# Optimization experiments

Hardware: AMD Instinct MI355X
Metric: run time of the kernel (lower is better)

The kernel has to match this reference:

```python
import jax, jax.numpy as jnp
import numpy as np

WS, OWS, NH, DIM, MLP_H = 16, 24, 6, 180, 360
PAD = (OWS - WS) // 2
SCALE = (DIM // NH) ** -0.5


def _ln(x, w, b):
    m = jnp.mean(x, -1, keepdims=True)
    v = jnp.var(x, -1, keepdims=True)
    return (x - m) * jax.lax.rsqrt(v + 1e-5) * w + b


def _rpi():
    # relative position index between ordinary (WS) and extended (OWS) windows
    ci = np.stack(np.meshgrid(np.arange(WS), np.arange(WS), indexing='ij')).reshape(2, -1)
    ce = np.stack(np.meshgrid(np.arange(OWS), np.arange(OWS), indexing='ij')).reshape(2, -1)
    rel = (ce[:, None, :] - ci[:, :, None]).transpose(1, 2, 0) + (WS - 1)  # [WS^2, OWS^2, 2]
    rel[:, :, 0] *= WS + OWS - 1
    return jnp.asarray(rel.sum(-1), dtype=jnp.int32)  # values in [0, (WS+OWS-1)^2)


def setup_inputs():
    key = jax.random.key(0)
    ks = jax.random.split(key, 8)
    h = w = 256
    b = 1
    p = lambda k, shape: jax.random.normal(k, shape, jnp.float32) * 0.02
    return {
        'x': jax.random.normal(ks[0], (b, h * w, DIM), jnp.float32),
        'rpi': _rpi(),
        'norm1_w': jnp.ones((DIM,), jnp.float32), 'norm1_b': jnp.zeros((DIM,), jnp.float32),
        'qkv_w': p(ks[1], (DIM, 3 * DIM)), 'qkv_b': jnp.zeros((3 * DIM,), jnp.float32),
        'rpb': p(ks[2], ((WS + OWS - 1) ** 2, NH)),
        'proj_w': p(ks[3], (DIM, DIM)), 'proj_b': jnp.zeros((DIM,), jnp.float32),
        'norm2_w': jnp.ones((DIM,), jnp.float32), 'norm2_b': jnp.zeros((DIM,), jnp.float32),
        'fc1_w': p(ks[4], (DIM, MLP_H)), 'fc1_b': jnp.zeros((MLP_H,), jnp.float32),
        'fc2_w': p(ks[5], (MLP_H, DIM)), 'fc2_b': jnp.zeros((DIM,), jnp.float32),
        'h': h, 'w': w,
    }


def _ocab(x, rpi, norm1_w, norm1_b, qkv_w, qkv_b, rpb, proj_w, proj_b,
          norm2_w, norm2_b, fc1_w, fc1_b, fc2_w, fc2_b, h, w):
    b, L, c = x.shape
    nhw, nww = h // WS, w // WS
    nw = nhw * nww
    shortcut = x
    xn = _ln(x, norm1_w, norm1_b).reshape(b, h, w, c)
    qkv = xn @ qkv_w + qkv_b                      # [b,h,w,3c]
    q = qkv[..., :c]
    kv = jnp.moveaxis(qkv[..., c:], -1, 1)        # [b,2c,h,w]
    # non-overlapping query windows -> [b*nw, WS*WS, c]
    qw = q.reshape(b, nhw, WS, nww, WS, c).transpose(0, 1, 3, 2, 4, 5).reshape(b * nw, WS * WS, c)
    # overlapping KV windows (torch.nn.Unfold(kernel=OWS, stride=WS, pad=PAD) equivalent)
    kv_pad = jnp.pad(kv, ((0, 0), (0, 0), (PAD, PAD), (PAD, PAD)))
    rows = (jnp.arange(nhw) * WS)[:, None] + jnp.arange(OWS)   # [nhw, OWS]
    cols = (jnp.arange(nww) * WS)[:, None] + jnp.arange(OWS)   # [nww, OWS]
    kvw = kv_pad[:, :, rows][:, :, :, :, cols]    # [b,2c,nhw,OWS,nww,OWS]
    kvw = kvw.reshape(b, 2, c, nhw, OWS, nww, OWS)
    kvw = kvw.transpose(1, 0, 3, 5, 4, 6, 2).reshape(2, b * nw, OWS * OWS, c)
    k_w, v_w = kvw[0], kvw[1]
    B_, nq, n, d = b * nw, WS * WS, OWS * OWS, c // NH
    q_ = qw.reshape(B_, nq, NH, d).transpose(0, 2, 1, 3) * SCALE
    k_ = k_w.reshape(B_, n, NH, d).transpose(0, 2, 1, 3)
    v_ = v_w.reshape(B_, n, NH, d).transpose(0, 2, 1, 3)
    attn = jnp.einsum('bhqd,bhnd->bhqn', q_, k_)
    bias = rpb[rpi.reshape(-1)].reshape(nq, n, NH).transpose(2, 0, 1)  # [NH, nq, n]
    attn = jax.nn.softmax(attn + bias[None], axis=-1)
    out = jnp.einsum('bhqn,bhnd->bhqd', attn, v_).transpose(0, 2, 1, 3).reshape(B_, nq, c)
    # window reverse
    out = out.reshape(b, nhw, nww, WS, WS, c).transpose(0, 1, 3, 2, 4, 5).reshape(b, h * w, c)
    x = out @ proj_w + proj_b + shortcut
    xn2 = _ln(x, norm2_w, norm2_b)
    mlp = jax.nn.gelu(xn2 @ fc1_w + fc1_b, approximate=False) @ fc2_w + fc2_b
    return x + mlp


def reference(x, rpi, norm1_w, norm1_b, qkv_w, qkv_b, rpb, proj_w, proj_b,
              norm2_w, norm2_b, fc1_w, fc1_b, fc2_w, fc2_b, h, w):
    return _ocab(x, rpi, norm1_w, norm1_b, qkv_w, qkv_b, rpb, proj_w, proj_b,
                 norm2_w, norm2_b, fc1_w, fc1_b, fc2_w, fc2_b, h, w)
```

## Files before the change

kernel.cpp:

```cpp
#include <hip/hip_runtime.h>

typedef float f32x4 __attribute__((ext_vector_type(4)));
typedef float fvec4 __attribute__((ext_vector_type(4)));
typedef __bf16 bf16x8 __attribute__((ext_vector_type(8)));
typedef unsigned short u16;
typedef u16 u16x8 __attribute__((ext_vector_type(8)));
typedef u16 u16x4 __attribute__((ext_vector_type(4)));
typedef int i32x2 __attribute__((ext_vector_type(2)));

#define SCALE_Q 0.18257418583505536f
#define LOG2E   1.4426950408889634f
#define SCALE_Q2 (SCALE_Q * LOG2E)

__device__ __forceinline__ u16 f2bf(float f) {
    union { __bf16 h; u16 u; } cv; cv.h = (__bf16)f; return cv.u;
}
__device__ __forceinline__ float bf2f(u16 u) {
    union { __bf16 h; u16 u; } cv; cv.u = u; return (float)cv.h;
}
__device__ __forceinline__ float exp2_raw(float x) {
    float r;
    asm("v_exp_f32 %0, %1" : "=v"(r) : "v"(x));
    return r;
}
__device__ __forceinline__ unsigned pk_bf16(float a, float b) {
    unsigned r;
    asm("v_cvt_pk_bf16_f32 %0, %1, %2" : "=v"(r) : "v"(a), "v"(b));
    return r;
}

#define GLD16(gsrc, ldst) __builtin_amdgcn_global_load_lds( \
    (const __attribute__((address_space(1))) unsigned*)(gsrc), \
    (__attribute__((address_space(3))) unsigned*)(ldst), 16, 0, 0)

__device__ __forceinline__ void xswap16(int a, int b, int& u, int& v) {
#if __has_builtin(__builtin_amdgcn_permlane16_swap)
    i32x2 r = __builtin_amdgcn_permlane16_swap(a, b, false, false);
    u = r[0]; v = r[1];
#else
    int sa = __builtin_amdgcn_ds_swizzle(a, 0x401F);
    int sb = __builtin_amdgcn_ds_swizzle(b, 0x401F);
    bool hi = (threadIdx.x & 16) != 0;
    u = hi ? sb : a;
    v = hi ? b : sa;
#endif
}

__device__ __forceinline__ void border_yx(int i, int& y, int& x) {
    if (i < 1056)      { y = i / 264; x = i % 264; }
    else if (i < 2112) { int j = i - 1056; y = 260 + j / 264; x = j % 264; }
    else               { int j = i - 2112; y = 4 + (j >> 3); int xx = j & 7;
                         x = (xx < 4) ? xx : 256 + xx; }
}

__global__ __launch_bounds__(256)
void prepln_k(const float* __restrict__ x, const float* __restrict__ n1w,
              const float* __restrict__ n1b, u16* __restrict__ xn,
              const float* __restrict__ qkv_w, const float* __restrict__ proj_w,
              const float* __restrict__ fc1_w, const float* __restrict__ fc2_w,
              const int* __restrict__ rpi, const float* __restrict__ rpb,
              u16* __restrict__ qkvT, u16* __restrict__ projT,
              u16* __restrict__ fc1T, u16* __restrict__ fc2T,
              u16* __restrict__ bias5, unsigned* __restrict__ kp_u32,
              unsigned* __restrict__ vp_u32)
{
    if (blockIdx.x < 16384) {
        int row = blockIdx.x * 4 + (threadIdx.x >> 6);
        int lane = threadIdx.x & 63;
        fvec4 v = {0.f, 0.f, 0.f, 0.f};
        if (lane < 45) v = *(const fvec4*)(x + (long)row * 180 + lane * 4);
        float s  = v.x + v.y + v.z + v.w;
        float sq = v.x * v.x + v.y * v.y + v.z * v.z + v.w * v.w;
        for (int m = 1; m < 64; m <<= 1) { s += __shfl_xor(s, m); sq += __shfl_xor(sq, m); }
        float mean = s * (1.f / 180.f);
        float var  = sq * (1.f / 180.f) - mean * mean;
        float rstd = rsqrtf(var + 1e-5f);
        if (lane < 45) {
            u16x4 o;
            #pragma unroll
            for (int j = 0; j < 4; j++) {
                int c = lane * 4 + j;
                o[j] = f2bf((v[j] - mean) * rstd * n1w[c] + n1b[c]);
            }
            *(u16x4*)(xn + (long)row * 192 + lane * 4) = o;
        } else if (lane < 48) {
            u16x4 z = {0, 0, 0, 0};
            *(u16x4*)(xn + (long)row * 192 + 180 + (lane - 45) * 4) = z;
        }
        return;
    }
    int idx = (blockIdx.x - 16384) * 256 + threadIdx.x;
    if (idx < 122880) {
        int e = idx & 7, l15b = (idx >> 3) & 15, lgb = (idx >> 7) & 3;
        int kstep = (idx >> 9) % 6, ng = idx / 3072;
        int col = ng * 16 + l15b, kd = kstep * 32 + lgb * 8 + e;
        qkvT[idx] = (col < 540 && kd < 180) ? f2bf(qkv_w[kd * 540 + col]) : (u16)0;
    } else if (idx < 172032) {
        int i = idx - 122880;
        int e = i & 7, l15b = (i >> 3) & 15, lgb = (i >> 7) & 3;
        int kstep = (i >> 9) % 6, ng = i / 3072;
        int col = ng * 16 + l15b, kdp = kstep * 32 + lgb * 8 + e;
        int sub = kdp & 31;
        int k = (kdp >> 5) * 30 + sub;
        projT[i] = (col < 180 && sub < 30) ? f2bf(proj_w[k * 180 + col]) : (u16)0;
    } else if (idx < 245760) {
        int i = idx - 172032;
        int e = i & 7, l15b = (i >> 3) & 15, lgb = (i >> 7) & 3;
        int kstep = (i >> 9) % 6, ng = i / 3072;
        int col = ng * 16 + l15b, kd = kstep * 32 + lgb * 8 + e;
        fc1T[i] = (col < 360 && kd < 180) ? f2bf(fc1_w[kd * 360 + col]) : (u16)0;
    } else if (idx < 344064) {
        int i = idx - 245760;
        int e = i & 7, l15b = (i >> 3) & 15, lgb = (i >> 7) & 3;
        int kstep = (i >> 9) % 12, ng = i / 6144;
        int col = ng * 16 + l15b, kd = kstep * 32 + lgb * 8 + e;
        fc2T[i] = (col < 180 && kd < 360) ? f2bf(fc2_w[kd * 180 + col]) : (u16)0;
    } else if (idx < 1228800) {
        int i = idx - 344064;
        int e = i & 15, l15 = (i >> 4) & 15, wv2 = (i >> 8) & 3, lg2 = (i >> 10) & 3;
        int cm36 = i >> 12;
        int hh = cm36 / 36, cm = cm36 % 36;
        int ch = cm >> 2, mi = cm & 3;
        int ni = e >> 2, rr = e & 3;
        int q = wv2 * 64 + ni * 16 + l15;
        int key = ch * 64 + mi * 16 + lg2 * 4 + rr;
        bias5[i] = f2bf(rpb[rpi[q * 576 + key] * 6 + hh] * LOG2E);
    } else if (idx < 1628160) {
        int i = idx - 1228800;
        int tok = i >> 4, wj = i & 15;
        int h = tok / 4160, b = tok % 4160, y, xx;
        border_yx(b, y, xx);
        kp_u32[((h * 264 + y) * 264 + xx) * 16 + wj] = 0u;
    } else if (idx < 2021376) {
        int i = idx - 1628160;
        int h = i / 65536, t = i % 65536;
        int y = t >> 8, xx = t & 255;
        kp_u32[((h * 264 + y + 4) * 264 + xx + 4) * 16 + 15] = 0u;
    } else if (idx < 2236800) {
        int i = idx - 2021376;
        int h = i / 35904, r = i % 35904;
        vp_u32[(h * 32 + 30) * 35904 + r] = 0x3F803F80u;
    } else if (idx < 2452224) {
        int i = idx - 2236800;
        int h = i / 35904, r = i % 35904;
        vp_u32[(h * 32 + 31) * 35904 + r] = 0u;
    } else if (idx < 3016704) {
        int i = idx - 2452224;
        int hd = i / 3136, j = i % 3136;
        int h = hd / 30, d = hd % 30;
        int y, xu;
        if (j < 1088) { int r = j / 136; y = r + (r >= 4 ? 256 : 0); xu = j % 136; }
        else { int j2 = j - 1088; y = 4 + (j2 >> 3); int q = j2 & 7;
               xu = (q < 2) ? q : 128 + q; }
        vp_u32[((h * 32 + d) * 264 + y) * 136 + xu] = 0u;
    }
}

template<int KTOT, int NCB, int EPI>
__global__ __launch_bounds__(256)
void gemm_k(const u16* __restrict__ A, const u16* __restrict__ BtF,
            const float* __restrict__ bias, const float* __restrict__ resid,
            void* __restrict__ o0, void* __restrict__ o1, void* __restrict__ o2)
{
    constexpr int NKT = KTOT / 32;
    __shared__ u16 lds_a[128 * 192];
    const int tid = threadIdx.x;
    const int l = tid & 63, wv = tid >> 6;
    const int wm = wv >> 1, wn = wv & 1;
    const int l15 = l & 15, lg = l >> 4;
    const int rx7 = l15 & 7;
    const long rowb = (long)blockIdx.x * 128;
    const int cb0 = blockIdx.y * NCB;
    const f32x4 fz = {0.f, 0.f, 0.f, 0.f};

    f32x4 acc[4][2];
    #pragma unroll
    for (int i = 0; i < 4; i++) { acc[i][0] = fz; acc[i][1] = fz; }

    const u16* aptr[4];
    #pragma unroll
    for (int mi = 0; mi < 4; mi++)
        aptr[mi] = lds_a + (wm * 64 + mi * 16 + l15) * 192;

    auto epilogue = [&](int cb, f32x4 (&ac)[4][2]) {
        #pragma unroll
        for (int nd = 0; nd < 2; nd++) {
            const int c = cb * 64 + wn * 32 + nd * 16 + l15;
            if (EPI == 0) {
                if (c < 540) {
                    const float bb = bias[c];
                    const int sec = (c >= 360) ? 2 : ((c >= 180) ? 1 : 0);
                    const int cc = c - sec * 180;
                    const int hh = cc / 30, d = cc - hh * 30;
                    #pragma unroll
                    for (int mi = 0; mi < 4; mi++) {
                        const long t0 = rowb + wm * 64 + mi * 16 + lg * 4;
                        const int y = (int)(t0 >> 8), x0 = (int)(t0 & 255);
                        if (sec == 0) {
                            int win = ((y >> 4) << 4) | (x0 >> 4);
                            int qrow0 = ((y & 15) << 4) | (x0 & 15);
                            u16* dst = (u16*)o0 + (((long)(win * 6 + hh)) * 256 + qrow0) * 32 + d;
                            #pragma unroll
                            for (int rr = 0; rr < 4; rr++)
                                dst[rr * 32] = f2bf((ac[mi][nd][rr] + bb) * SCALE_Q2);
                        } else if (sec == 1) {
                            u16* dst = (u16*)o1 + (((long)hh * 264 + y + 4) * 264 + x0 + 4) * 32 + d;
                            #pragma unroll
                            for (int rr = 0; rr < 4; rr++)
                                dst[rr * 32] = f2bf(ac[mi][nd][rr] + bb);
                        } else {
                            long dstoff = (((long)hh * 32 + d) * 264 + y + 4) * 272 + x0 + 4;
                            union { u16x4 v4; unsigned u2[2]; } pv;
                            pv.u2[0] = pk_bf16(ac[mi][nd][0] + bb, ac[mi][nd][1] + bb);
                            pv.u2[1] = pk_bf16(ac[mi][nd][2] + bb, ac[mi][nd][3] + bb);
                            *(u16x4*)((u16*)o2 + dstoff) = pv.v4;
                        }
                    }
                }
            } else {
                if (c < 180) {
                    const float bb = bias[c];
                    #pragma unroll
                    for (int mi = 0; mi < 4; mi++) {
                        const long t0 = rowb + wm * 64 + mi * 16 + lg * 4;
                        const float* rs = resid + t0 * 180 + c;
                        u16* dst = (u16*)o0 + t0 * 192 + c;
                        #pragma unroll
                        for (int rr = 0; rr < 4; rr++)
                            dst[rr * 192] = f2bf(ac[mi][nd][rr] + bb + rs[rr * 180]);
                    }
                } else {
                    #pragma unroll
                    for (int mi = 0; mi < 4; mi++) {
                        const long t0 = rowb + wm * 64 + mi * 16 + lg * 4;
                        u16* dst = (u16*)o0 + t0 * 192 + c;
                        #pragma unroll
                        for (int rr = 0; rr < 4; rr++)
                            dst[rr * 192] = 0;
                    }
                }
            }
        }
    };

    #pragma unroll
    for (int R = 0; R < 12; ++R) {
        int idx = R * 256 + tid;
        int row = idx / 24, gp = idx - row * 24;
        int g = (gp & 24) | ((gp & 7) ^ (row & 7));
        GLD16(A + (rowb + row) * KTOT + g * 8,
              (char*)lds_a + R * 4096 + wv * 1024);
    }
    __syncthreads();

    #pragma unroll
    for (int icb = 0; icb < NCB; ++icb) {
        const u16* Bf = BtF + ((long)((cb0 + icb) * 4 + wn * 2) * NKT) * 512 + l * 8;
        #pragma unroll
        for (int kg = 0; kg < 6; kg += 3) {
            bf16x8 bfr[2][3];
            #pragma unroll
            for (int g2 = 0; g2 < 3; ++g2) {
                bfr[0][g2] = *(const bf16x8*)(Bf + (kg + g2) * 512);
                bfr[1][g2] = *(const bf16x8*)(Bf + (NKT + kg + g2) * 512);
            }
            #pragma unroll
            for (int g2 = 0; g2 < 3; ++g2) {
                const int k = kg + g2;
                const int gk = k * 4 + lg;
                const int gpk = (gk & 24) | ((gk & 7) ^ rx7);
                bf16x8 af[4];
                #pragma unroll
                for (int mi = 0; mi < 4; mi++)
                    af[mi] = *(const bf16x8*)(aptr[mi] + gpk * 8);
                #pragma unroll
                for (int mi = 0; mi < 4; mi++)
                    #pragma unroll
                    for (int nd = 0; nd < 2; nd++)
                        acc[mi][nd] = __builtin_amdgcn_mfma_f32_16x16x32_bf16(af[mi], bfr[nd][g2], acc[mi][nd], 0, 0, 0);
            }
        }
        epilogue(cb0 + icb, acc);
        #pragma unroll
        for (int i = 0; i < 4; i++) { acc[i][0] = fz; acc[i][1] = fz; }
    }
}

__global__ __launch_bounds__(256)
void mlp_k(const u16* __restrict__ x2b, const u16* __restrict__ fc1T,
           const u16* __restrict__ fc2T, const float* __restrict__ b1,
           const float* __restrict__ b2, const float* __restrict__ n2w,
           const float* __restrict__ n2b, float* __restrict__ out)
{
    __shared__ u16 lds_a[64 * 192];
    __shared__ u16 H[64 * 384];
    const int tid = threadIdx.x;
    const int l = tid & 63, wv = tid >> 6;
    const int l15 = l & 15, lg = l >> 4;
    const int rx7 = l15 & 7;
    const long rowb = (long)blockIdx.x * 64;
    const f32x4 fz = {0.f, 0.f, 0.f, 0.f};

    #pragma unroll
    for (int R = 0; R < 6; ++R) {
        int idx = R * 256 + tid;
        int row = idx / 24, gp = idx - row * 24;
        int g = (gp & 24) | ((gp & 7) ^ (row & 7));
        GLD16(x2b + (rowb + row) * 192 + g * 8, (char*)lds_a + R * 4096 + wv * 1024);
    }
    __syncthreads();

    {
        const int row = tid >> 2, q = tid & 3;
        const int rw7 = row & 7;
        u16* rbase = lds_a + row * 192;
        u16x8 vals[6];
        float s = 0.f, sq = 0.f;
        #pragma unroll
        for (int j = 0; j < 6; ++j) {
            int g = q * 6 + j;
            int pg = (g & 24) | ((g & 7) ^ rw7);
            vals[j] = *(const u16x8*)(rbase + pg * 8);
            #pragma unroll
            for (int e = 0; e < 8; ++e) {
                float v = bf2f(vals[j][e]);
                s += v; sq += v * v;
            }
        }
        s  += __shfl_xor(s, 1);  sq += __shfl_xor(sq, 1);
        s  += __shfl_xor(s, 2);  sq += __shfl_xor(sq, 2);
        float mean = s * (1.f / 180.f);
        float var  = sq * (1.f / 180.f) - mean * mean;
        float rstd = rsqrtf(var + 1e-5f);
        #pragma unroll
        for (int j = 0; j < 6; ++j) {
            int g = q * 6 + j;
            int pg = (g & 24) | ((g & 7) ^ rw7);
            u16x8 o;
            #pragma unroll
            for (int e = 0; e < 8; ++e) {
                int c = g * 8 + e;
                int cc = (c < 180) ? c : 0;
                float v = bf2f(vals[j][e]);
                float nv = (v - mean) * rstd * n2w[cc] + n2b[cc];
                o[e] = (c < 180) ? f2bf(nv) : (u16)0;
            }
            *(u16x8*)(rbase + pg * 8) = o;
        }
    }
    __syncthreads();

    const u16* aptr[4];
    #pragma unroll
    for (int mi = 0; mi < 4; mi++)
        aptr[mi] = lds_a + (mi * 16 + l15) * 192;

    #pragma unroll
    for (int cb = 0; cb < 6; ++cb) {
        f32x4 ac[4] = {fz, fz, fz, fz};
        const u16* Bf = fc1T + ((long)(cb * 4 + wv) * 6) * 512 + l * 8;
        #pragma unroll
        for (int k = 0; k < 6; ++k) {
            bf16x8 bfr = *(const bf16x8*)(Bf + k * 512);
            const int gk = k * 4 + lg;
            const int gpk = (gk & 24) | ((gk & 7) ^ rx7);
            bf16x8 af[4];
            #pragma unroll
            for (int mi = 0; mi < 4; mi++)
                af[mi] = *(const bf16x8*)(aptr[mi] + gpk * 8);
            #pragma unroll
            for (int mi = 0; mi < 4; mi++)
                ac[mi] = __builtin_amdgcn_mfma_f32_16x16x32_bf16(af[mi], bfr, ac[mi], 0, 0, 0);
        }
        const int c = cb * 64 + wv * 16 + l15;
        const float bb = (c < 360) ? b1[c] : 0.f;
        const int gC = c >> 3, cL = c & 7;
        #pragma unroll
        for (int mi = 0; mi < 4; mi++) {
            #pragma unroll
            for (int rr = 0; rr < 4; rr++) {
                int row = mi * 16 + lg * 4 + rr;
                float xx = ac[mi][rr] + bb;
                float u2n = -2.f * xx * (0.7978845608f + 0.0356774081f * xx * xx);
                float ge = xx / (1.f + __expf(u2n));
                int gS = (gC & ~7) | ((gC & 7) ^ (row & 7));
                H[row * 384 + gS * 8 + cL] = f2bf(ge);
            }
        }
    }
    __syncthreads();

    #pragma unroll
    for (int cb = 0; cb < 3; ++cb) {
        f32x4 ac[4] = {fz, fz, fz, fz};
        const u16* Bf = fc2T + ((long)(cb * 4 + wv) * 12) * 512 + l * 8;
        #pragma unroll
        for (int k = 0; k < 12; ++k) {
            bf16x8 bfr = *(const bf16x8*)(Bf + k * 512);
            const int gk = k * 4 + lg;
            const int gS = (gk & ~7) | ((gk & 7) ^ rx7);
            bf16x8 af[4];
            #pragma unroll
            for (int mi = 0; mi < 4; mi++)
                af[mi] = *(const bf16x8*)(H + (mi * 16 + l15) * 384 + gS * 8);
            #pragma unroll
            for (int mi = 0; mi < 4; mi++)
                ac[mi] = __builtin_amdgcn_mfma_f32_16x16x32_bf16(af[mi], bfr, ac[mi], 0, 0, 0);
        }
        const int c = cb * 64 + wv * 16 + l15;
        if (c < 180) {
            const float bb = b2[c];
            #pragma unroll
            for (int mi = 0; mi < 4; mi++) {
                const long t0 = rowb + mi * 16 + lg * 4;
                const u16* rs = x2b + t0 * 192 + c;
                float* dst = out + t0 * 180 + c;
                #pragma unroll
                for (int rr = 0; rr < 4; rr++)
                    dst[rr * 180] = ac[mi][rr] + bb + bf2f(rs[rr * 192]);
            }
        }
    }
}

__global__ __launch_bounds__(256)
void attn_k(const u16* __restrict__ q_g, const u16* __restrict__ K_pad,
            const u16* __restrict__ vP, const u16* __restrict__ bias5,
            u16* __restrict__ attn_out)
{
    __shared__ u16 kc[2][64 * 32];
    __shared__ u16 vt[2][32 * 64];

    const int w = ((blockIdx.x & 7) << 5) | (blockIdx.x >> 3);
    const int h = blockIdx.y;
    const int wy = w >> 4, wx = w & 15;
    const int tid = threadIdx.x;
    const int wv = tid >> 6, l = tid & 63;
    const int l15 = l & 15, lg = l >> 4;
    const int swzk = (l15 >> 1) & 3;
    const int swzv = l15 & 7;

    bf16x8 qb[4];
    #pragma unroll
    for (int ni = 0; ni < 4; ni++) {
        int qrow = wv * 64 + ni * 16 + l15;
        qb[ni] = *(const bf16x8*)(q_g + (((long)(w * 6 + h)) * 256 + qrow) * 32 + lg * 8);
    }

    f32x4 acc[2][4];
    #pragma unroll
    for (int i = 0; i < 2; i++)
        #pragma unroll
        for (int j = 0; j < 4; j++) acc[i][j] = (f32x4){0.f, 0.f, 0.f, 0.f};

    const int tK = tid >> 2;
    const int gtk = (l & 3) ^ ((l >> 3) & 3);
    const int aK = (tK >= 48) ? 2 : (tK >= 24 ? 1 : 0);
    const int bK = tK - aK * 24;
    const u16* KbaseRow = K_pad + (((long)(h * 264 + wy * 16)) * 264 + wx * 16) * 32 + gtk * 8;
    const int dV = tid >> 3;
    const int gtv = (l & 7) ^ (l >> 3);
    const int aV = gtv / 3, bV = (gtv % 3) * 8;
    const u16* Vrow0 = vP + ((((long)h * 32 + dV) * 264) + wy * 16) * 272 + wx * 16;
    const u16* Bp = bias5 + (long)h * 147456 + ((lg * 4 + wv) * 16 + l15) * 16;

    GLD16(KbaseRow + ((long)aK * 264 + bK) * 32, (char*)kc[0] + wv * 1024);
    GLD16(Vrow0 + aV * 272 + bV, (char*)vt[0] + wv * 1024);

    u16x8 bl[4], bh[4];
    #pragma unroll
    for (int mi = 0; mi < 4; mi++) {
        bl[mi] = *(const u16x8*)(Bp + mi * 4096);
        bh[mi] = *(const u16x8*)(Bp + mi * 4096 + 8);
    }

    #pragma unroll
    for (int ch = 0; ch < 9; ++ch) {
        __syncthreads();
        u16x8 bln[4], bhn[4];
        if (ch < 8) {
            int n = (ch + 1) * 64;
            int c1 = n / 24, c2 = n - c1 * 24;
            int bb2 = bK + c2;
            int t2 = bb2 >= 24;
            int oy = c1 + aK + t2, ox = bb2 - (t2 ? 24 : 0);
            GLD16(KbaseRow + ((long)oy * 264 + ox) * 32, (char*)kc[(ch + 1) & 1] + wv * 1024);
            int bbv = bV + c2;
            int t2v = bbv >= 24;
            int oyv = c1 + aV + t2v, oxv = bbv - (t2v ? 24 : 0);
            GLD16(Vrow0 + oyv * 272 + oxv, (char*)vt[(ch + 1) & 1] + wv * 1024);
            #pragma unroll
            for (int mi = 0; mi < 4; mi++) {
                bln[mi] = *(const u16x8*)(Bp + ((ch + 1) * 4 + mi) * 4096);
                bhn[mi] = *(const u16x8*)(Bp + ((ch + 1) * 4 + mi) * 4096 + 8);
            }
        }
        const u16* kcur = kc[ch & 1];
        const u16* vcur = vt[ch & 1];

        #pragma unroll
        for (int ks = 0; ks < 2; ++ks) {
            int Wp[2][4][2];
            #pragma unroll
            for (int mih = 0; mih < 2; ++mih) {
                int mi = ks * 2 + mih;
                int key = ks * 32 + mih * 16 + l15;
                bf16x8 ka = *(const bf16x8*)(kcur + key * 32 + (lg ^ swzk) * 8);
                union { u16x8 v; unsigned d[4]; } ulo, uhi;
                ulo.v = bl[mi]; uhi.v = bh[mi];
                f32x4 s[4];
                #pragma unroll
                for (int ni = 0; ni < 4; ni++) {
                    unsigned dA = (ni < 2) ? ulo.d[(ni & 1) * 2]     : uhi.d[(ni & 1) * 2];
                    unsigned dB = (ni < 2) ? ulo.d[(ni & 1) * 2 + 1] : uhi.d[(ni & 1) * 2 + 1];
                    f32x4 ci;
                    ci[0] = __uint_as_float(dA << 16);
                    ci[1] = __uint_as_float(dA & 0xFFFF0000u);
                    ci[2] = __uint_as_float(dB << 16);
                    ci[3] = __uint_as_float(dB & 0xFFFF0000u);
                    s[ni] = ci;
                }
                #pragma unroll
                for (int ni = 0; ni < 4; ni++)
                    s[ni] = __builtin_amdgcn_mfma_f32_16x16x32_bf16(ka, qb[ni], s[ni], 0, 0, 0);
                #pragma unroll
                for (int ni = 0; ni < 4; ni++) {
                    float p0 = exp2_raw(s[ni][0]);
                    float p1 = exp2_raw(s[ni][1]);
                    float p2 = exp2_raw(s[ni][2]);
                    float p3 = exp2_raw(s[ni][3]);
                    Wp[mih][ni][0] = (int)pk_bf16(p0, p1);
                    Wp[mih][ni][1] = (int)pk_bf16(p2, p3);
                }
            }
            bf16x8 va0 = *(const bf16x8*)(vcur + l15 * 64 + ((ks * 4 + lg) ^ swzv) * 8);
            bf16x8 va1 = *(const bf16x8*)(vcur + (16 + l15) * 64 + ((ks * 4 + lg) ^ swzv) * 8);
            #pragma unroll
            for (int ni = 0; ni < 4; ni++) {
                i32x2 r0 = __builtin_amdgcn_permlane32_swap(Wp[0][ni][0], Wp[1][ni][0], false, false);
                i32x2 r1 = __builtin_amdgcn_permlane32_swap(Wp[0][ni][1], Wp[1][ni][1], false, false);
                int wd0, wd1, wd2, wd3;
                xswap16(r0[0], r0[1], wd0, wd2);
                xswap16(r1[0], r1[1], wd1, wd3);
                union { int wd[4]; bf16x8 v; } pu;
                pu.wd[0] = wd0; pu.wd[1] = wd1; pu.wd[2] = wd2; pu.wd[3] = wd3;
                acc[0][ni] = __builtin_amdgcn_mfma_f32_16x16x32_bf16(va0, pu.v, acc[0][ni], 0, 0, 0);
                acc[1][ni] = __builtin_amdgcn_mfma_f32_16x16x32_bf16(va1, pu.v, acc[1][ni], 0, 0, 0);
            }
        }
        if (ch < 8) {
            #pragma unroll
            for (int mi = 0; mi < 4; mi++) { bl[mi] = bln[mi]; bh[mi] = bhn[mi]; }
        }
    }

    #pragma unroll
    for (int ni = 0; ni < 4; ni++) {
        float sum = __shfl(acc[1][ni][2], 48 + l15);
        float inv = 1.f / sum;
        int q = wv * 64 + ni * 16 + l15;
        int y = wy * 16 + (q >> 4), x = wx * 16 + (q & 15);
        u16* bp = attn_out + ((long)(y * 256 + x)) * 192 + h * 32;
        *(unsigned*)(bp + lg * 4)     = pk_bf16(acc[0][ni][0] * inv, acc[0][ni][1] * inv);
        *(unsigned*)(bp + lg * 4 + 2) = pk_bf16(acc[0][ni][2] * inv, acc[0][ni][3] * inv);
        if (lg < 3) {
            *(unsigned*)(bp + 16 + lg * 4)     = pk_bf16(acc[1][ni][0] * inv, acc[1][ni][1] * inv);
            *(unsigned*)(bp + 16 + lg * 4 + 2) = pk_bf16(acc[1][ni][2] * inv, acc[1][ni][3] * inv);
        } else {
            *(unsigned*)(bp + 28) = pk_bf16(acc[1][ni][0] * inv, acc[1][ni][1] * inv);
            *(unsigned*)(bp + 30) = 0u;
        }
    }
}

extern "C" void kernel_launch(void* const* d_in, const int* in_sizes, int n_in,
                              void* d_out, int out_size, void* d_ws, size_t ws_size,
                              hipStream_t stream)
{
    (void)in_sizes; (void)n_in; (void)out_size; (void)ws_size;
    const float* x      = (const float*)d_in[0];
    const int*   rpi    = (const int*)d_in[1];
    const float* n1w    = (const float*)d_in[2];
    const float* n1b    = (const float*)d_in[3];
    const float* qkv_w  = (const float*)d_in[4];
    const float* qkv_b  = (const float*)d_in[5];
    const float* rpb    = (const float*)d_in[6];
    const float* proj_w = (const float*)d_in[7];
    const float* proj_b = (const float*)d_in[8];
    const float* n2w    = (const float*)d_in[9];
    const float* n2b    = (const float*)d_in[10];
    const float* fc1_w  = (const float*)d_in[11];
    const float* fc1_b  = (const float*)d_in[12];
    const float* fc2_w  = (const float*)d_in[13];
    const float* fc2_b  = (const float*)d_in[14];
    float* out = (float*)d_out;

    char* ws = (char*)d_ws;
    size_t off = 0;
    auto alloc = [&](size_t bytes) -> void* {
        void* p = ws + off; off += (bytes + 511) & ~(size_t)511; return p;
    };
    u16*   xn     = (u16*)alloc(65536ull * 192 * 2);
    u16*   q_g    = (u16*)alloc(65536ull * 192 * 2);
    u16*   K_pad  = (u16*)alloc(6ull * 264 * 264 * 32 * 2);
    u16*   x2b    = (u16*)alloc(65536ull * 192 * 2);
    u16*   vP     = (u16*)alloc(6ull * 32 * 264 * 272 * 2);
    u16*   bias5  = (u16*)alloc(6ull * 36 * 4 * 4 * 16 * 16 * 2);
    u16*   qkvT   = (u16*)alloc(640ull * 192 * 2);
    u16*   projT  = (u16*)alloc(256ull * 192 * 2);
    u16*   fc1T   = (u16*)alloc(384ull * 192 * 2);
    u16*   fc2T   = (u16*)alloc(256ull * 384 * 2);
    u16*   ao     = xn;

    prepln_k<<<dim3(28168), dim3(256), 0, stream>>>(x, n1w, n1b, xn,
        qkv_w, proj_w, fc1_w, fc2_w, rpi, rpb,
        qkvT, projT, fc1T, fc2T, bias5, (unsigned*)K_pad, (unsigned*)vP);
    gemm_k<192, 3, 0><<<dim3(512, 3), dim3(256), 0, stream>>>(
        xn, qkvT, qkv_b, (const float*)nullptr, q_g, K_pad, vP);
    attn_k<<<dim3(256, 6), dim3(256), 0, stream>>>(q_g, K_pad, vP, bias5, ao);
    gemm_k<192, 3, 1><<<dim3(512, 1), dim3(256), 0, stream>>>(
        ao, projT, proj_b, x, x2b, nullptr, nullptr);
    mlp_k<<<dim3(1024), dim3(256), 0, stream>>>(
        x2b, fc1T, fc2T, fc1_b, fc2_b, n2w, n2b, out);
}
```

Measured before the change: 209.9 us.

## Split MLP hidden dim into halves and stage two KV chunks per barrier

The MLP kernel now computes the fc1+GELU hidden activations in two 192-wide halves and accumulates fc2 partial products into persistent registers. This halves the H shared buffer, which may allow more resident blocks, at the cost of an extra barrier and more accumulator registers. The attention kernel now loads two 64-key K/V chunks per stage into doubled LDS buffers. This halves the number of __syncthreads in the chunk loop, but bias prefetching is dropped and bias is now loaded inline per chunk, and LDS use in attn_k grows.

```diff
diff --git a/kernel.cpp b/kernel.cpp
--- a/kernel.cpp
+++ b/kernel.cpp
@@ -293,7 +293,7 @@
            const float* __restrict__ n2b, float* __restrict__ out)
 {
     __shared__ u16 lds_a[64 * 192];
-    __shared__ u16 H[64 * 384];
+    __shared__ u16 H[64 * 192];
     const int tid = threadIdx.x;
     const int l = tid & 63, wv = tid >> 6;
     const int l15 = l & 15, lg = l >> 4;
@@ -355,58 +355,72 @@
     for (int mi = 0; mi < 4; mi++)
         aptr[mi] = lds_a + (mi * 16 + l15) * 192;
 
-    #pragma unroll
-    for (int cb = 0; cb < 6; ++cb) {
-        f32x4 ac[4] = {fz, fz, fz, fz};
-        const u16* Bf = fc1T + ((long)(cb * 4 + wv) * 6) * 512 + l * 8;
-        #pragma unroll
-        for (int k = 0; k < 6; ++k) {
-            bf16x8 bfr = *(const bf16x8*)(Bf + k * 512);
-            const int gk = k * 4 + lg;
-            const int gpk = (gk & 24) | ((gk & 7) ^ rx7);
-            bf16x8 af[4];
-            #pragma unroll
-            for (int mi = 0; mi < 4; mi++)
-                af[mi] = *(const bf16x8*)(aptr[mi] + gpk * 8);
-            #pragma unroll
-            for (int mi = 0; mi < 4; mi++)
-                ac[mi] = __builtin_amdgcn_mfma_f32_16x16x32_bf16(af[mi], bfr, ac[mi], 0, 0, 0);
-        }
-        const int c = cb * 64 + wv * 16 + l15;
-        const float bb = (c < 360) ? b1[c] : 0.f;
-        const int gC = c >> 3, cL = c & 7;
-        #pragma unroll
-        for (int mi = 0; mi < 4; mi++) {
-            #pragma unroll
-            for (int rr = 0; rr < 4; rr++) {
-                int row = mi * 16 + lg * 4 + rr;
-                float xx = ac[mi][rr] + bb;
-                float u2n = -2.f * xx * (0.7978845608f + 0.0356774081f * xx * xx);
-                float ge = xx / (1.f + __expf(u2n));
-                int gS = (gC & ~7) | ((gC & 7) ^ (row & 7));
-                H[row * 384 + gS * 8 + cL] = f2bf(ge);
-            }
-        }
-    }
-    __syncthreads();
+    f32x4 acc2[3][4];
+    #pragma unroll
+    for (int cb = 0; cb < 3; ++cb)
+        #pragma unroll
+        for (int mi = 0; mi < 4; mi++) acc2[cb][mi] = fz;
+
+    #pragma unroll
+    for (int hk = 0; hk < 2; ++hk) {
+        if (hk) __syncthreads();
+        #pragma unroll
+        for (int cb = 0; cb < 3; ++cb) {
+            const int cbg = hk * 3 + cb;
+            f32x4 ac[4] = {fz, fz, fz, fz};
+            const u16* Bf = fc1T + ((long)(cbg * 4 + wv) * 6) * 512 + l * 8;
+            #pragma unroll
+            for (int k = 0; k < 6; ++k) {
+                bf16x8 bfr = *(const bf16x8*)(Bf + k * 512);
+                const int gk = k * 4 + lg;
+                const int gpk = (gk & 24) | ((gk & 7) ^ rx7);
+                bf16x8 af[4];
+                #pragma unroll
+                for (int mi = 0; mi < 4; mi++)
+                    af[mi] = *(const bf16x8*)(aptr[mi] + gpk * 8);
+                #pragma unroll
+                for (int mi = 0; mi < 4; mi++)
+                    ac[mi] = __builtin_amdgcn_mfma_f32_16x16x32_bf16(af[mi], bfr, ac[mi], 0, 0, 0);
+            }
+            const int cg = cbg * 64 + wv * 16 + l15;
+            const int cl = cb * 64 + wv * 16 + l15;
+            const float bb = (cg < 360) ? b1[cg] : 0.f;
+            const int gC = cl >> 3, cL = cl & 7;
+            #pragma unroll
+            for (int mi = 0; mi < 4; mi++) {
+                #pragma unroll
+                for (int rr = 0; rr < 4; rr++) {
+                    int row = mi * 16 + lg * 4 + rr;
+                    float xx = ac[mi][rr] + bb;
+                    float u2n = -2.f * xx * (0.7978845608f + 0.0356774081f * xx * xx);
+                    float ge = xx / (1.f + __expf(u2n));
+                    int gS = (gC & ~7) | ((gC & 7) ^ (row & 7));
+                    H[row * 192 + gS * 8 + cL] = f2bf(ge);
+                }
+            }
+        }
+        __syncthreads();
+        #pragma unroll
+        for (int cb = 0; cb < 3; ++cb) {
+            const u16* Bf = fc2T + ((long)(cb * 4 + wv) * 12 + hk * 6) * 512 + l * 8;
+            #pragma unroll
+            for (int k = 0; k < 6; ++k) {
+                bf16x8 bfr = *(const bf16x8*)(Bf + k * 512);
+                const int gk = k * 4 + lg;
+                const int gS = (gk & 24) | ((gk & 7) ^ rx7);
+                bf16x8 af[4];
+                #pragma unroll
+                for (int mi = 0; mi < 4; mi++)
+                    af[mi] = *(const bf16x8*)(H + (mi * 16 + l15) * 192 + gS * 8);
+                #pragma unroll
+                for (int mi = 0; mi < 4; mi++)
+                    acc2[cb][mi] = __builtin_amdgcn_mfma_f32_16x16x32_bf16(af[mi], bfr, acc2[cb][mi], 0, 0, 0);
+            }
+        }
+    }
 
     #pragma unroll
     for (int cb = 0; cb < 3; ++cb) {
-        f32x4 ac[4] = {fz, fz, fz, fz};
-        const u16* Bf = fc2T + ((long)(cb * 4 + wv) * 12) * 512 + l * 8;
-        #pragma unroll
-        for (int k = 0; k < 12; ++k) {
-            bf16x8 bfr = *(const bf16x8*)(Bf + k * 512);
-            const int gk = k * 4 + lg;
-            const int gS = (gk & ~7) | ((gk & 7) ^ rx7);
-            bf16x8 af[4];
-            #pragma unroll
-            for (int mi = 0; mi < 4; mi++)
-                af[mi] = *(const bf16x8*)(H + (mi * 16 + l15) * 384 + gS * 8);
-            #pragma unroll
-            for (int mi = 0; mi < 4; mi++)
-                ac[mi] = __builtin_amdgcn_mfma_f32_16x16x32_bf16(af[mi], bfr, ac[mi], 0, 0, 0);
-        }
         const int c = cb * 64 + wv * 16 + l15;
         if (c < 180) {
             const float bb = b2[c];
@@ -417,7 +431,7 @@
                 float* dst = out + t0 * 180 + c;
                 #pragma unroll
                 for (int rr = 0; rr < 4; rr++)
-                    dst[rr * 180] = ac[mi][rr] + bb + bf2f(rs[rr * 192]);
+                    dst[rr * 180] = acc2[cb][mi][rr] + bb + bf2f(rs[rr * 192]);
             }
         }
     }
@@ -428,8 +442,8 @@
             const u16* __restrict__ vP, const u16* __restrict__ bias5,
             u16* __restrict__ attn_out)
 {
-    __shared__ u16 kc[2][64 * 32];
-    __shared__ u16 vt[2][32 * 64];
+    __shared__ u16 kc[2][128 * 32];
+    __shared__ u16 vt[2][128 * 32];
 
     const int w = ((blockIdx.x & 7) << 5) | (blockIdx.x >> 3);
     const int h = blockIdx.y;
@@ -464,93 +478,92 @@
     const u16* Vrow0 = vP + ((((long)h * 32 + dV) * 264) + wy * 16) * 272 + wx * 16;
     const u16* Bp = bias5 + (long)h * 147456 + ((lg * 4 + wv) * 16 + l15) * 16;
 
-    GLD16(KbaseRow + ((long)aK * 264 + bK) * 32, (char*)kc[0] + wv * 1024);
-    GLD16(Vrow0 + aV * 272 + bV, (char*)vt[0] + wv * 1024);
-
-    u16x8 bl[4], bh[4];
-    #pragma unroll
-    for (int mi = 0; mi < 4; mi++) {
-        bl[mi] = *(const u16x8*)(Bp + mi * 4096);
-        bh[mi] = *(const u16x8*)(Bp + mi * 4096 + 8);
-    }
-
-    #pragma unroll
-    for (int ch = 0; ch < 9; ++ch) {
+    auto stageKV = [&](int cc, int buf, int s) {
+        int n = cc * 64;
+        int c1 = n / 24, c2 = n - c1 * 24;
+        int bb2 = bK + c2;
+        int t2 = bb2 >= 24;
+        int oy = c1 + aK + t2, ox = bb2 - (t2 ? 24 : 0);
+        GLD16(KbaseRow + ((long)oy * 264 + ox) * 32,
+              (char*)kc[buf] + s * 4096 + wv * 1024);
+        int bbv = bV + c2;
+        int t2v = bbv >= 24;
+        int oyv = c1 + aV + t2v, oxv = bbv - (t2v ? 24 : 0);
+        GLD16(Vrow0 + oyv * 272 + oxv,
+              (char*)vt[buf] + s * 4096 + wv * 1024);
+    };
+
+    stageKV(0, 0, 0);
+    stageKV(1, 0, 1);
+
+    #pragma unroll
+    for (int r = 0; r < 5; ++r) {
         __syncthreads();
-        u16x8 bln[4], bhn[4];
-        if (ch < 8) {
-            int n = (ch + 1) * 64;
-            int c1 = n / 24, c2 = n - c1 * 24;
-            int bb2 = bK + c2;
-            int t2 = bb2 >= 24;
-            int oy = c1 + aK + t2, ox = bb2 - (t2 ? 24 : 0);
-            GLD16(KbaseRow + ((long)oy * 264 + ox) * 32, (char*)kc[(ch + 1) & 1] + wv * 1024);
-            int bbv = bV + c2;
-            int t2v = bbv >= 24;
-            int oyv = c1 + aV + t2v, oxv = bbv - (t2v ? 24 : 0);
-            GLD16(Vrow0 + oyv * 272 + oxv, (char*)vt[(ch + 1) & 1] + wv * 1024);
+        if (2 * r + 2 < 9) stageKV(2 * r + 2, (r + 1) & 1, 0);
+        if (2 * r + 3 < 9) stageKV(2 * r + 3, (r + 1) & 1, 1);
+
+        #pragma unroll
+        for (int s = 0; s < 2; ++s) {
+            const int cc = 2 * r + s;
+            if (cc >= 9) break;
+            const u16* kcur = kc[r & 1] + s * 2048;
+            const u16* vcur = vt[r & 1] + s * 2048;
+            u16x8 bl[4], bh[4];
             #pragma unroll
             for (int mi = 0; mi < 4; mi++) {
-                bln[mi] = *(const u16x8*)(Bp + ((ch + 1) * 4 + mi) * 4096);
-                bhn[mi] = *(const u16x8*)(Bp + ((ch + 1) * 4 + mi) * 4096 + 8);
-            }
-        }
-        const u16* kcur = kc[ch & 1];
-        const u16* vcur = vt[ch & 1];
-
-        #pragma unroll
-        for (int ks = 0; ks < 2; ++ks) {
-            int Wp[2][4][2];
-            #pragma unroll
-            for (int mih = 0; mih < 2; ++mih) {
-                int mi = ks * 2 + mih;
-                int key = ks * 32 + mih * 16 + l15;
-                bf16x8 ka = *(const bf16x8*)(kcur + key * 32 + (lg ^ swzk) * 8);
-                union { u16x8 v; unsigned d[4]; } ulo, uhi;
-                ulo.v = bl[mi]; uhi.v = bh[mi];
-                f32x4 s[4];
+                bl[mi] = *(const u16x8*)(Bp + (cc * 4 + mi) * 4096);
+                bh[mi] = *(const u16x8*)(Bp + (cc * 4 + mi) * 4096 + 8);
+            }
+            #pragma unroll
+            for (int ks = 0; ks < 2; ++ks) {
+                int Wp[2][4][2];
+                #pragma unroll
+                for (int mih = 0; mih < 2; ++mih) {
+                    int mi = ks * 2 + mih;
+                    int key = ks * 32 + mih * 16 + l15;
+                    bf16x8 ka = *(const bf16x8*)(kcur + key * 32 + (lg ^ swzk) * 8);
+                    union { u16x8 v; unsigned d[4]; } ulo, uhi;
+                    ulo.v = bl[mi]; uhi.v = bh[mi];
+                    f32x4 ss[4];
+                    #pragma unroll
+                    for (int ni = 0; ni < 4; ni++) {
+                        unsigned dA = (ni < 2) ? ulo.d[(ni & 1) * 2]     : uhi.d[(ni & 1) * 2];
+                        unsigned dB = (ni < 2) ? ulo.d[(ni & 1) * 2 + 1] : uhi.d[(ni & 1) * 2 + 1];
+                        f32x4 ci;
+                        ci[0] = __uint_as_float(dA << 16);
+                        ci[1] = __uint_as_float(dA & 0xFFFF0000u);
+                        ci[2] = __uint_as_float(dB << 16);
+                        ci[3] = __uint_as_float(dB & 0xFFFF0000u);
+                        ss[ni] = ci;
+                    }
+                    #pragma unroll
+                    for (int ni = 0; ni < 4; ni++)
+                        ss[ni] = __builtin_amdgcn_mfma_f32_16x16x32_bf16(ka, qb[ni], ss[ni], 0, 0, 0);
+                    #pragma unroll
+                    for (int ni = 0; ni < 4; ni++) {
+                        float p0 = exp2_raw(ss[ni][0]);
+                        float p1 = exp2_raw(ss[ni][1]);
+                        float p2 = exp2_raw(ss[ni][2]);
+                        float p3 = exp2_raw(ss[ni][3]);
+                        Wp[mih][ni][0] = (int)pk_bf16(p0, p1);
+                        Wp[mih][ni][1] = (int)pk_bf16(p2, p3);
+                    }
+                }
+                bf16x8 va0 = *(const bf16x8*)(vcur + l15 * 64 + ((ks * 4 + lg) ^ swzv) * 8);
+                bf16x8 va1 = *(const bf16x8*)(vcur + (16 + l15) * 64 + ((ks * 4 + lg) ^ swzv) * 8);
                 #pragma unroll
                 for (int ni = 0; ni < 4; ni++) {
-                    unsigned dA = (ni < 2) ? ulo.d[(ni & 1) * 2]     : uhi.d[(ni & 1) * 2];
-                    unsigned dB = (ni < 2) ? ulo.d[(ni & 1) * 2 + 1] : uhi.d[(ni & 1) * 2 + 1];
-                    f32x4 ci;
-                    ci[0] = __uint_as_float(dA << 16);
-                    ci[1] = __uint_as_float(dA & 0xFFFF0000u);
-                    ci[2] = __uint_as_float(dB << 16);
-                    ci[3] = __uint_as_float(dB & 0xFFFF0000u);
-                    s[ni] = ci;
+                    i32x2 r0 = __builtin_amdgcn_permlane32_swap(Wp[0][ni][0], Wp[1][ni][0], false, false);
+                    i32x2 r1 = __builtin_amdgcn_permlane32_swap(Wp[0][ni][1], Wp[1][ni][1], false, false);
+                    int wd0, wd1, wd2, wd3;
+                    xswap16(r0[0], r0[1], wd0, wd2);
+                    xswap16(r1[0], r1[1], wd1, wd3);
+                    union { int wd[4]; bf16x8 v; } pu;
+                    pu.wd[0] = wd0; pu.wd[1] = wd1; pu.wd[2] = wd2; pu.wd[3] = wd3;
+                    acc[0][ni] = __builtin_amdgcn_mfma_f32_16x16x32_bf16(va0, pu.v, acc[0][ni], 0, 0, 0);
+                    acc[1][ni] = __builtin_amdgcn_mfma_f32_16x16x32_bf16(va1, pu.v, acc[1][ni], 0, 0, 0);
                 }
-                #pragma unroll
-                for (int ni = 0; ni < 4; ni++)
-                    s[ni] = __builtin_amdgcn_mfma_f32_16x16x32_bf16(ka, qb[ni], s[ni], 0, 0, 0);
-                #pragma unroll
-                for (int ni = 0; ni < 4; ni++) {
-                    float p0 = exp2_raw(s[ni][0]);
-                    float p1 = exp2_raw(s[ni][1]);
-                    float p2 = exp2_raw(s[ni][2]);
-                    float p3 = exp2_raw(s[ni][3]);
-                    Wp[mih][ni][0] = (int)pk_bf16(p0, p1);
-                    Wp[mih][ni][1] = (int)pk_bf16(p2, p3);
-                }
-            }
-            bf16x8 va0 = *(const bf16x8*)(vcur + l15 * 64 + ((ks * 4 + lg) ^ swzv) * 8);
-            bf16x8 va1 = *(const bf16x8*)(vcur + (16 + l15) * 64 + ((ks * 4 + lg) ^ swzv) * 8);
-            #pragma unroll
-            for (int ni = 0; ni < 4; ni++) {
-                i32x2 r0 = __builtin_amdgcn_permlane32_swap(Wp[0][ni][0], Wp[1][ni][0], false, false);
-                i32x2 r1 = __builtin_amdgcn_permlane32_swap(Wp[0][ni][1], Wp[1][ni][1], false, false);
-                int wd0, wd1, wd2, wd3;
-                xswap16(r0[0], r0[1], wd0, wd2);
-                xswap16(r1[0], r1[1], wd1, wd3);
-                union { int wd[4]; bf16x8 v; } pu;
-                pu.wd[0] = wd0; pu.wd[1] = wd1; pu.wd[2] = wd2; pu.wd[3] = wd3;
-                acc[0][ni] = __builtin_amdgcn_mfma_f32_16x16x32_bf16(va0, pu.v, acc[0][ni], 0, 0, 0);
-                acc[1][ni] = __builtin_amdgcn_mfma_f32_16x16x32_bf16(va1, pu.v, acc[1][ni], 0, 0, 0);
-            }
-        }
-        if (ch < 8) {
-            #pragma unroll
-            for (int mi = 0; mi < 4; mi++) { bl[mi] = bln[mi]; bh[mi] = bhn[mi]; }
+            }
         }
     }
 
```

New measurement: 239.6 us. +14.1%, slower.

## Fuse output projection and residual add into the MLP kernel

Applied to the files above, without the earlier changes.

Drops the separate projection GEMM launch and computes attn_out@proj_w + bias + shortcut inside mlp_k. The result is written straight to LDS as the LN2/fc1 input, and the residual is kept in registers for the final add. This removes the x2b global round trip and one kernel launch. In exchange, LDS is repartitioned into three 64x192 buffers with the GELU hidden tile split across two of them, and register pressure rises from holding the residual.

```diff
diff --git a/kernel.cpp b/kernel.cpp
--- a/kernel.cpp
+++ b/kernel.cpp
@@ -156,10 +156,10 @@
     }
 }
 
-template<int KTOT, int NCB, int EPI>
+template<int KTOT, int NCB>
 __global__ __launch_bounds__(256)
 void gemm_k(const u16* __restrict__ A, const u16* __restrict__ BtF,
-            const float* __restrict__ bias, const float* __restrict__ resid,
+            const float* __restrict__ bias,
             void* __restrict__ o0, void* __restrict__ o1, void* __restrict__ o2)
 {
     constexpr int NKT = KTOT / 32;
@@ -186,57 +186,33 @@
         #pragma unroll
         for (int nd = 0; nd < 2; nd++) {
             const int c = cb * 64 + wn * 32 + nd * 16 + l15;
-            if (EPI == 0) {
-                if (c < 540) {
-                    const float bb = bias[c];
-                    const int sec = (c >= 360) ? 2 : ((c >= 180) ? 1 : 0);
-                    const int cc = c - sec * 180;
-                    const int hh = cc / 30, d = cc - hh * 30;
-                    #pragma unroll
-                    for (int mi = 0; mi < 4; mi++) {
-                        const long t0 = rowb + wm * 64 + mi * 16 + lg * 4;
-                        const int y = (int)(t0 >> 8), x0 = (int)(t0 & 255);
-                        if (sec == 0) {
-                            int win = ((y >> 4) << 4) | (x0 >> 4);
-                            int qrow0 = ((y & 15) << 4) | (x0 & 15);
-                            u16* dst = (u16*)o0 + (((long)(win * 6 + hh)) * 256 + qrow0) * 32 + d;
-                            #pragma unroll
-                            for (int rr = 0; rr < 4; rr++)
-                                dst[rr * 32] = f2bf((ac[mi][nd][rr] + bb) * SCALE_Q2);
-                        } else if (sec == 1) {
-                            u16* dst = (u16*)o1 + (((long)hh * 264 + y + 4) * 264 + x0 + 4) * 32 + d;
-                            #pragma unroll
-                            for (int rr = 0; rr < 4; rr++)
-                                dst[rr * 32] = f2bf(ac[mi][nd][rr] + bb);
-                        } else {
-                            long dstoff = (((long)hh * 32 + d) * 264 + y + 4) * 272 + x0 + 4;
-                            union { u16x4 v4; unsigned u2[2]; } pv;
-                            pv.u2[0] = pk_bf16(ac[mi][nd][0] + bb, ac[mi][nd][1] + bb);
-                            pv.u2[1] = pk_bf16(ac[mi][nd][2] + bb, ac[mi][nd][3] + bb);
-                            *(u16x4*)((u16*)o2 + dstoff) = pv.v4;
-                        }
-                    }
-                }
-            } else {
-                if (c < 180) {
-                    const float bb = bias[c];
-                    #pragma unroll
-                    for (int mi = 0; mi < 4; mi++) {
-                        const long t0 = rowb + wm * 64 + mi * 16 + lg * 4;
-                        const float* rs = resid + t0 * 180 + c;
-                        u16* dst = (u16*)o0 + t0 * 192 + c;
+            if (c < 540) {
+                const float bb = bias[c];
+                const int sec = (c >= 360) ? 2 : ((c >= 180) ? 1 : 0);
+                const int cc = c - sec * 180;
+                const int hh = cc / 30, d = cc - hh * 30;
+                #pragma unroll
+                for (int mi = 0; mi < 4; mi++) {
+                    const long t0 = rowb + wm * 64 + mi * 16 + lg * 4;
+                    const int y = (int)(t0 >> 8), x0 = (int)(t0 & 255);
+                    if (sec == 0) {
+                        int win = ((y >> 4) << 4) | (x0 >> 4);
+                        int qrow0 = ((y & 15) << 4) | (x0 & 15);
+                        u16* dst = (u16*)o0 + (((long)(win * 6 + hh)) * 256 + qrow0) * 32 + d;
                         #pragma unroll
                         for (int rr = 0; rr < 4; rr++)
-                            dst[rr * 192] = f2bf(ac[mi][nd][rr] + bb + rs[rr * 180]);
-                    }
-                } else {
-                    #pragma unroll
-                    for (int mi = 0; mi < 4; mi++) {
-                        const long t0 = rowb + wm * 64 + mi * 16 + lg * 4;
-                        u16* dst = (u16*)o0 + t0 * 192 + c;
+                            dst[rr * 32] = f2bf((ac[mi][nd][rr] + bb) * SCALE_Q2);
+                    } else if (sec == 1) {
+                        u16* dst = (u16*)o1 + (((long)hh * 264 + y + 4) * 264 + x0 + 4) * 32 + d;
                         #pragma unroll
                         for (int rr = 0; rr < 4; rr++)
-                            dst[rr * 192] = 0;
+                            dst[rr * 32] = f2bf(ac[mi][nd][rr] + bb);
+                    } else {
+                        long dstoff = (((long)hh * 32 + d) * 264 + y + 4) * 272 + x0 + 4;
+                        union { u16x4 v4; unsigned u2[2]; } pv;
+                        pv.u2[0] = pk_bf16(ac[mi][nd][0] + bb, ac[mi][nd][1] + bb);
+                        pv.u2[1] = pk_bf16(ac[mi][nd][2] + bb, ac[mi][nd][3] + bb);
+                        *(u16x4*)((u16*)o2 + dstoff) = pv.v4;
                     }
                 }
             }
@@ -287,13 +263,16 @@
 }
 
 __global__ __launch_bounds__(256)
-void mlp_k(const u16* __restrict__ x2b, const u16* __restrict__ fc1T,
-           const u16* __restrict__ fc2T, const float* __restrict__ b1,
-           const float* __restrict__ b2, const float* __restrict__ n2w,
-           const float* __restrict__ n2b, float* __restrict__ out)
+void mlp_k(const u16* __restrict__ ao, const u16* __restrict__ projT,
+           const u16* __restrict__ fc1T, const u16* __restrict__ fc2T,
+           const float* __restrict__ pb, const float* __restrict__ b1,
+           const float* __restrict__ b2, const float* __restrict__ xres,
+           const float* __restrict__ n2w, const float* __restrict__ n2b,
+           float* __restrict__ out)
 {
-    __shared__ u16 lds_a[64 * 192];
-    __shared__ u16 H[64 * 384];
+    __shared__ u16 buf0[64 * 192];
+    __shared__ u16 x2bL[64 * 192];
+    __shared__ u16 buf2[64 * 192];
     const int tid = threadIdx.x;
     const int l = tid & 63, wv = tid >> 6;
     const int l15 = l & 15, lg = l >> 4;
@@ -306,14 +285,63 @@
         int idx = R * 256 + tid;
         int row = idx / 24, gp = idx - row * 24;
         int g = (gp & 24) | ((gp & 7) ^ (row & 7));
-        GLD16(x2b + (rowb + row) * 192 + g * 8, (char*)lds_a + R * 4096 + wv * 1024);
+        GLD16(ao + (rowb + row) * 192 + g * 8, (char*)buf0 + R * 4096 + wv * 1024);
+    }
+    __syncthreads();
+
+    const u16* aptr0[4];
+    #pragma unroll
+    for (int mi = 0; mi < 4; mi++)
+        aptr0[mi] = buf0 + (mi * 16 + l15) * 192;
+
+    unsigned resid[3][4][2];
+    #pragma unroll
+    for (int cb = 0; cb < 3; ++cb) {
+        f32x4 ac[4] = {fz, fz, fz, fz};
+        const u16* Bf = projT + ((long)(cb * 4 + wv) * 6) * 512 + l * 8;
+        #pragma unroll
+        for (int k = 0; k < 6; ++k) {
+            bf16x8 bfr = *(const bf16x8*)(Bf + k * 512);
+            const int gk = k * 4 + lg;
+            const int gpk = (gk & 24) | ((gk & 7) ^ rx7);
+            bf16x8 af[4];
+            #pragma unroll
+            for (int mi = 0; mi < 4; mi++)
+                af[mi] = *(const bf16x8*)(aptr0[mi] + gpk * 8);
+            #pragma unroll
+            for (int mi = 0; mi < 4; mi++)
+                ac[mi] = __builtin_amdgcn_mfma_f32_16x16x32_bf16(af[mi], bfr, ac[mi], 0, 0, 0);
+        }
+        const int c = cb * 64 + wv * 16 + l15;
+        const bool valid = (c < 180);
+        const float bb = valid ? pb[c] : 0.f;
+        const int g = c >> 3, e = c & 7;
+        #pragma unroll
+        for (int mi = 0; mi < 4; mi++) {
+            const long t0 = rowb + mi * 16 + lg * 4;
+            float v[4];
+            #pragma unroll
+            for (int rr = 0; rr < 4; rr++)
+                v[rr] = valid ? (ac[mi][rr] + bb + xres[(t0 + rr) * 180 + c]) : 0.f;
+            unsigned p0 = pk_bf16(v[0], v[1]);
+            unsigned p1 = pk_bf16(v[2], v[3]);
+            resid[cb][mi][0] = p0;
+            resid[cb][mi][1] = p1;
+            #pragma unroll
+            for (int rr = 0; rr < 4; rr++) {
+                int row = mi * 16 + lg * 4 + rr;
+                int gS = (g & 24) | ((g & 7) ^ (row & 7));
+                unsigned pw = (rr < 2) ? p0 : p1;
+                x2bL[row * 192 + gS * 8 + e] = (u16)((pw >> ((rr & 1) * 16)) & 0xFFFF);
+            }
+        }
     }
     __syncthreads();
 
     {
         const int row = tid >> 2, q = tid & 3;
         const int rw7 = row & 7;
-        u16* rbase = lds_a + row * 192;
+        u16* rbase = x2bL + row * 192;
         u16x8 vals[6];
         float s = 0.f, sq = 0.f;
         #pragma unroll
@@ -353,7 +381,7 @@
     const u16* aptr[4];
     #pragma unroll
     for (int mi = 0; mi < 4; mi++)
-        aptr[mi] = lds_a + (mi * 16 + l15) * 192;
+        aptr[mi] = x2bL + (mi * 16 + l15) * 192;
 
     #pragma unroll
     for (int cb = 0; cb < 6; ++cb) {
@@ -374,7 +402,9 @@
         }
         const int c = cb * 64 + wv * 16 + l15;
         const float bb = (c < 360) ? b1[c] : 0.f;
-        const int gC = c >> 3, cL = c & 7;
+        u16* Hb = (cb < 3) ? buf0 : buf2;
+        const int cl = (cb < 3 ? cb : cb - 3) * 64 + wv * 16 + l15;
+        const int gC = cl >> 3, cL = cl & 7;
         #pragma unroll
         for (int mi = 0; mi < 4; mi++) {
             #pragma unroll
@@ -384,7 +414,7 @@
                 float u2n = -2.f * xx * (0.7978845608f + 0.0356774081f * xx * xx);
                 float ge = xx / (1.f + __expf(u2n));
                 int gS = (gC & ~7) | ((gC & 7) ^ (row & 7));
-                H[row * 384 + gS * 8 + cL] = f2bf(ge);
+                Hb[row * 192 + gS * 8 + cL] = f2bf(ge);
             }
         }
     }
@@ -397,12 +427,13 @@
         #pragma unroll
         for (int k = 0; k < 12; ++k) {
             bf16x8 bfr = *(const bf16x8*)(Bf + k * 512);
-            const int gk = k * 4 + lg;
-            const int gS = (gk & ~7) | ((gk & 7) ^ rx7);
+            const u16* Hb = (k < 6) ? buf0 : buf2;
+            const int gk2 = (k < 6 ? k : k - 6) * 4 + lg;
+            const int gS = (gk2 & ~7) | ((gk2 & 7) ^ rx7);
             bf16x8 af[4];
             #pragma unroll
             for (int mi = 0; mi < 4; mi++)
-                af[mi] = *(const bf16x8*)(H + (mi * 16 + l15) * 384 + gS * 8);
+                af[mi] = *(const bf16x8*)(Hb + (mi * 16 + l15) * 192 + gS * 8);
             #pragma unroll
             for (int mi = 0; mi < 4; mi++)
                 ac[mi] = __builtin_amdgcn_mfma_f32_16x16x32_bf16(af[mi], bfr, ac[mi], 0, 0, 0);
@@ -413,11 +444,13 @@
             #pragma unroll
             for (int mi = 0; mi < 4; mi++) {
                 const long t0 = rowb + mi * 16 + lg * 4;
-                const u16* rs = x2b + t0 * 192 + c;
                 float* dst = out + t0 * 180 + c;
                 #pragma unroll
-                for (int rr = 0; rr < 4; rr++)
-                    dst[rr * 180] = ac[mi][rr] + bb + bf2f(rs[rr * 192]);
+                for (int rr = 0; rr < 4; rr++) {
+                    unsigned pw = resid[cb][mi][rr >> 1];
+                    u16 rb = (u16)((pw >> ((rr & 1) * 16)) & 0xFFFF);
+                    dst[rr * 180] = ac[mi][rr] + bb + bf2f(rb);
+                }
             }
         }
     }
@@ -603,7 +636,6 @@
     u16*   xn     = (u16*)alloc(65536ull * 192 * 2);
     u16*   q_g    = (u16*)alloc(65536ull * 192 * 2);
     u16*   K_pad  = (u16*)alloc(6ull * 264 * 264 * 32 * 2);
-    u16*   x2b    = (u16*)alloc(65536ull * 192 * 2);
     u16*   vP     = (u16*)alloc(6ull * 32 * 264 * 272 * 2);
     u16*   bias5  = (u16*)alloc(6ull * 36 * 4 * 4 * 16 * 16 * 2);
     u16*   qkvT   = (u16*)alloc(640ull * 192 * 2);
@@ -615,11 +647,9 @@
     prepln_k<<<dim3(28168), dim3(256), 0, stream>>>(x, n1w, n1b, xn,
         qkv_w, proj_w, fc1_w, fc2_w, rpi, rpb,
         qkvT, projT, fc1T, fc2T, bias5, (unsigned*)K_pad, (unsigned*)vP);
-    gemm_k<192, 3, 0><<<dim3(512, 3), dim3(256), 0, stream>>>(
-        xn, qkvT, qkv_b, (const float*)nullptr, q_g, K_pad, vP);
+    gemm_k<192, 3><<<dim3(512, 3), dim3(256), 0, stream>>>(
+        xn, qkvT, qkv_b, q_g, K_pad, vP);
     attn_k<<<dim3(256, 6), dim3(256), 0, stream>>>(q_g, K_pad, vP, bias5, ao);
-    gemm_k<192, 3, 1><<<dim3(512, 1), dim3(256), 0, stream>>>(
-        ao, projT, proj_b, x, x2b, nullptr, nullptr);
     mlp_k<<<dim3(1024), dim3(256), 0, stream>>>(
-        x2b, fc1T, fc2T, fc1_b, fc2_b, n2w, n2b, out);
-}
+        ao, projT, fc1T, fc2T, proj_b, fc1_b, fc2_b, x, n2w, n2b, out);
+}
```

Measured after the change: 277.8 us. 1.32x slower.
